# Optimization experiments

Measured on AMD Instinct MI355X. Metric: run time of the kernel, lower is better.

Reference implementation:

```python
import jax, jax.numpy as jnp
import numpy as np
import math

NUM_FILTERS = 128
SAMPLE_RATE = 16000
N_FFT = 2048
FREQ_MIN, FREQ_MAX = 20.0, 8000.0


def setup_inputs() -> dict:
    key = jax.random.key(0)
    B, FB, T = 32, N_FFT // 2 + 1, 2000
    spectrum = jax.random.normal(key, (B, FB, T), dtype=jnp.float32)
    # mel-scale init of center frequencies (in FFT-bin units), as in __init__
    mel_min = 2595.0 * math.log10(1.0 + FREQ_MIN / 700.0)
    mel_max = 2595.0 * math.log10(1.0 + FREQ_MAX / 700.0)
    mel_points = jnp.linspace(mel_min, mel_max, NUM_FILTERS, dtype=jnp.float32)
    freq_points = 700.0 * (10.0 ** (mel_points / 2595.0) - 1.0)
    center_freqs = freq_points * N_FFT / SAMPLE_RATE  # [F]
    bandwidths = jnp.full((NUM_FILTERS,), N_FFT / NUM_FILTERS / 4.0, dtype=jnp.float32)
    filter_shapes = jnp.ones((NUM_FILTERS, 2), dtype=jnp.float32)
    return {"spectrum": spectrum, "center_freqs": center_freqs,
            "bandwidths": bandwidths, "filter_shapes": filter_shapes}


def _build_filterbank(center_freqs, bandwidths, filter_shapes, freq_bins):
    # Vectorized over all filters: [F, freq_bins]
    freqs = jnp.arange(freq_bins, dtype=jnp.float32)[None, :]        # [1, K]
    center = center_freqs[:, None]                                    # [F, 1]
    bw = (jax.nn.softplus(bandwidths) + 0.001)[:, None]               # [F, 1]
    slopes = jax.nn.softplus(filter_shapes) + 0.1                     # [F, 2]
    left_edge = center - bw * slopes[:, 0:1]
    right_edge = center + bw * slopes[:, 1:2]
    rise = (freqs >= left_edge) & (freqs <= center)
    fall = (freqs > center) & (freqs <= right_edge)
    resp = jnp.where(rise, (freqs - left_edge) / (center - left_edge + 1e-8), 0.0)
    resp = jnp.where(fall, 1.0 - (freqs - center) / (right_edge - center + 1e-8), resp)
    return resp  # [F, K]


def reference(spectrum, center_freqs, bandwidths, filter_shapes):
    B, K, T = spectrum.shape
    F = center_freqs.shape[0]
    filterbank = _build_filterbank(center_freqs, bandwidths, filter_shapes, K)
    # [F, K] x [B, K, T] -> [B, F, T]
    filtered = jnp.einsum('fk,bkt->bft', filterbank, spectrum)
    # Faithful to original: reshape [B, F, T] -> [F, B, T], then permute(1,2,0) -> [B, T, F]
    filtered = filtered.reshape(F, B, T)
    return jnp.transpose(filtered, (1, 2, 0))
```

## Files before the change

### kernel.cpp

```cpp
#include <hip/hip_runtime.h>

#define K_BINS 1025
#define T_LEN  2000
#define NF     128
#define TQ     500

__device__ __forceinline__ float softplusf(float x) {
    return fmaxf(x, 0.0f) + log1pf(expf(-fabsf(x)));
}

__global__ __launch_bounds__(1024) void fb_fused(
        const float* __restrict__ spec,
        const float* __restrict__ cf,
        const float* __restrict__ bwv,
        const float* __restrict__ fs,
        float*       __restrict__ out) {
    const int q    = blockIdx.x;
    const int B    = blockIdx.y;
    const int th   = blockIdx.z;
    const int tid  = threadIdx.x;
    const int lane = tid & 63;
    const int wid  = tid >> 6;
    const int w    = wid >> 2;
    const int p    = wid & 3;
    const int bp   = 4 * q + p;
    const int t0   = TQ * th;

    float lef[4], cen[4], icl[4], irc[4];
    int   klo[4], khi[4];
#pragma unroll
    for (int i = 0; i < 4; ++i) {
        const int f = 4 * B + 32 * w + i;
        float c  = cf[f];
        float bw = softplusf(bwv[f]) + 0.001f;
        float s0 = softplusf(fs[2 * f])     + 0.1f;
        float s1 = softplusf(fs[2 * f + 1]) + 0.1f;
        float left  = c - bw * s0;
        float right = c + bw * s1;
        lef[i] = left;
        cen[i] = c;
        icl[i] = 1.0f / (c - left + 1e-8f);
        irc[i] = 1.0f / (right - c + 1e-8f);
        klo[i] = max(0, (int)ceilf(left));
        khi[i] = min(K_BINS - 1, (int)floorf(right));
    }
    const int klo_u = min(min(klo[0], klo[1]), min(klo[2], klo[3]));
    const int khi_u = max(max(khi[0], khi[1]), max(khi[2], khi[3]));

    float4 acc[4][2];
#pragma unroll
    for (int i = 0; i < 4; ++i) {
        acc[i][0] = make_float4(0.f, 0.f, 0.f, 0.f);
        acc[i][1] = make_float4(0.f, 0.f, 0.f, 0.f);
    }

    const float* base = spec + (size_t)bp * (K_BINS * (size_t)T_LEN) + t0;
    const bool ok1 = (64 + lane) < (TQ / 4);

    for (int k = klo_u; k <= khi_u; ++k) {
        float fk = (float)k;
        float wg[4];
        float wm = 0.0f;
#pragma unroll
        for (int i = 0; i < 4; ++i) {
            float rise = (fk - lef[i]) * icl[i];
            float fall = fmaf(-(fk - cen[i]), irc[i], 1.0f);
            wg[i] = fmaxf(0.0f, fminf(rise, fall));
            wm = fmaxf(wm, wg[i]);
        }
        if (wm > 0.0f) {
            const float4* rp = (const float4*)(base + (size_t)k * T_LEN);
            float4 v0 = rp[lane];
            float4 v1 = make_float4(0.f, 0.f, 0.f, 0.f);
            if (ok1) v1 = rp[64 + lane];
#pragma unroll
            for (int i = 0; i < 4; ++i) {
                acc[i][0].x = fmaf(wg[i], v0.x, acc[i][0].x);
                acc[i][0].y = fmaf(wg[i], v0.y, acc[i][0].y);
                acc[i][0].z = fmaf(wg[i], v0.z, acc[i][0].z);
                acc[i][0].w = fmaf(wg[i], v0.w, acc[i][0].w);
                acc[i][1].x = fmaf(wg[i], v1.x, acc[i][1].x);
                acc[i][1].y = fmaf(wg[i], v1.y, acc[i][1].y);
                acc[i][1].z = fmaf(wg[i], v1.z, acc[i][1].z);
                acc[i][1].w = fmaf(wg[i], v1.w, acc[i][1].w);
            }
        }
    }

    __shared__ float tile[512][17];
#pragma unroll
    for (int i = 0; i < 4; ++i) {
        __syncthreads();
        {
            const int col = 4 * p + w;
            const int r0  = 4 * lane;
#pragma unroll
            for (int r = 0; r < 4; ++r)
                tile[r0 + r][col] = (&acc[i][0].x)[r];
            if (ok1) {
                const int r1 = 256 + 4 * lane;
#pragma unroll
                for (int r = 0; r < 4; ++r)
                    tile[r1 + r][col] = (&acc[i][1].x)[r];
            }
        }
        __syncthreads();
        const int b2 = 4 * B + i;
        const int c4 = tid & 3;
#pragma unroll
        for (int rr = 0; rr < 2; ++rr) {
            int tl = 256 * rr + (tid >> 2);
            if (tl < TQ) {
                float4 v = make_float4(tile[tl][4 * c4 + 0], tile[tl][4 * c4 + 1],
                                       tile[tl][4 * c4 + 2], tile[tl][4 * c4 + 3]);
                *reinterpret_cast<float4*>(
                    out + ((size_t)b2 * T_LEN + t0 + tl) * NF + 16 * q + 4 * c4) = v;
            }
        }
    }
}

extern "C" void kernel_launch(void* const* d_in, const int* in_sizes, int n_in,
                              void* d_out, int out_size, void* d_ws, size_t ws_size,
                              hipStream_t stream) {
    const float* spec = (const float*)d_in[0];
    const float* cf   = (const float*)d_in[1];
    const float* bwv  = (const float*)d_in[2];
    const float* fs   = (const float*)d_in[3];
    float* out = (float*)d_out;

    fb_fused<<<dim3(8, 8, 4), 1024, 0, stream>>>(spec, cf, bwv, fs, out);
}
```

Baseline: 62.38 us.

## Prefetch next spectrum row and iterate only merged filter support ranges

The k loop now walks a list of merged contiguous bin ranges covering the four filters' supports, so it no longer computes weights for bins that fall in gaps between them. It software-pipelines the loop by loading the next row's float4 values while the FMAs for the current row run, which hides global memory latency. The weight computation is folded into precomputed affine coefficients, saving a subtraction per filter. The costs are more live registers for the prefetched values, and the old per-bin zero-weight skip is gone, so bins inside a merged range that have zero weight still get loaded.

Result: no change. 61.91 us (-0.7%).

```diff
diff --git a/kernel.cpp b/kernel.cpp
--- a/kernel.cpp
+++ b/kernel.cpp
@@ -26,7 +26,7 @@
     const int bp   = 4 * q + p;
     const int t0   = TQ * th;
 
-    float lef[4], cen[4], icl[4], irc[4];
+    float icl[4], irc[4], Af[4], Bf[4];
     int   klo[4], khi[4];
 #pragma unroll
     for (int i = 0; i < 4; ++i) {
@@ -37,15 +37,24 @@
         float s1 = softplusf(fs[2 * f + 1]) + 0.1f;
         float left  = c - bw * s0;
         float right = c + bw * s1;
-        lef[i] = left;
-        cen[i] = c;
         icl[i] = 1.0f / (c - left + 1e-8f);
         irc[i] = 1.0f / (right - c + 1e-8f);
+        Af[i]  = left * icl[i];
+        Bf[i]  = fmaf(c, irc[i], 1.0f);
         klo[i] = max(0, (int)ceilf(left));
         khi[i] = min(K_BINS - 1, (int)floorf(right));
     }
-    const int klo_u = min(min(klo[0], klo[1]), min(klo[2], klo[3]));
-    const int khi_u = max(max(khi[0], khi[1]), max(khi[2], khi[3]));
+
+    int rs[4], re[4], nr = 0;
+    {
+        int cs = klo[0], ce = khi[0];
+#pragma unroll
+        for (int i = 1; i < 4; ++i) {
+            if (klo[i] <= ce + 1) ce = max(ce, khi[i]);
+            else { rs[nr] = cs; re[nr] = ce; ++nr; cs = klo[i]; ce = khi[i]; }
+        }
+        rs[nr] = cs; re[nr] = ce; ++nr;
+    }
 
     float4 acc[4][2];
 #pragma unroll
@@ -54,37 +63,46 @@
         acc[i][1] = make_float4(0.f, 0.f, 0.f, 0.f);
     }
 
-    const float* base = spec + (size_t)bp * (K_BINS * (size_t)T_LEN) + t0;
+    const float4* base4 =
+        (const float4*)(spec + (size_t)bp * (K_BINS * (size_t)T_LEN) + t0);
     const bool ok1 = (64 + lane) < (TQ / 4);
 
-    for (int k = klo_u; k <= khi_u; ++k) {
-        float fk = (float)k;
-        float wg[4];
-        float wm = 0.0f;
+    int rcur = 0;
+    int kcur = rs[0];
+    float4 v0 = base4[(size_t)kcur * 500 + lane];
+    float4 v1 = make_float4(0.f, 0.f, 0.f, 0.f);
+    if (ok1) v1 = base4[(size_t)kcur * 500 + 64 + lane];
+
+    while (kcur >= 0) {
+        int knext, rnext = rcur;
+        if (kcur + 1 <= re[rcur])      knext = kcur + 1;
+        else if (rcur + 1 < nr)        { rnext = rcur + 1; knext = rs[rnext]; }
+        else                           knext = -1;
+
+        float4 n0, n1;
+        if (knext >= 0) {
+            const float4* np = base4 + (size_t)knext * 500;
+            n0 = np[lane];
+            if (ok1) n1 = np[64 + lane];
+        }
+
+        float fk = (float)kcur;
 #pragma unroll
         for (int i = 0; i < 4; ++i) {
-            float rise = (fk - lef[i]) * icl[i];
-            float fall = fmaf(-(fk - cen[i]), irc[i], 1.0f);
-            wg[i] = fmaxf(0.0f, fminf(rise, fall));
-            wm = fmaxf(wm, wg[i]);
+            float rise = fmaf(fk, icl[i], -Af[i]);
+            float fall = fmaf(-fk, irc[i], Bf[i]);
+            float wg   = fmaxf(0.0f, fminf(rise, fall));
+            acc[i][0].x = fmaf(wg, v0.x, acc[i][0].x);
+            acc[i][0].y = fmaf(wg, v0.y, acc[i][0].y);
+            acc[i][0].z = fmaf(wg, v0.z, acc[i][0].z);
+            acc[i][0].w = fmaf(wg, v0.w, acc[i][0].w);
+            acc[i][1].x = fmaf(wg, v1.x, acc[i][1].x);
+            acc[i][1].y = fmaf(wg, v1.y, acc[i][1].y);
+            acc[i][1].z = fmaf(wg, v1.z, acc[i][1].z);
+            acc[i][1].w = fmaf(wg, v1.w, acc[i][1].w);
         }
-        if (wm > 0.0f) {
-            const float4* rp = (const float4*)(base + (size_t)k * T_LEN);
-            float4 v0 = rp[lane];
-            float4 v1 = make_float4(0.f, 0.f, 0.f, 0.f);
-            if (ok1) v1 = rp[64 + lane];
-#pragma unroll
-            for (int i = 0; i < 4; ++i) {
-                acc[i][0].x = fmaf(wg[i], v0.x, acc[i][0].x);
-                acc[i][0].y = fmaf(wg[i], v0.y, acc[i][0].y);
-                acc[i][0].z = fmaf(wg[i], v0.z, acc[i][0].z);
-                acc[i][0].w = fmaf(wg[i], v0.w, acc[i][0].w);
-                acc[i][1].x = fmaf(wg[i], v1.x, acc[i][1].x);
-                acc[i][1].y = fmaf(wg[i], v1.y, acc[i][1].y);
-                acc[i][1].z = fmaf(wg[i], v1.z, acc[i][1].z);
-                acc[i][1].w = fmaf(wg[i], v1.w, acc[i][1].w);
-            }
-        }
+        v0 = n0; v1 = n1;
+        kcur = knext; rcur = rnext;
     }
 
     __shared__ float tile[512][17];
```
